# Kernel tuning notes

Measured on AMD Instinct MI355X. Metric: run time of the kernel, lower is better.

Reference implementation:

```python
import jax, jax.numpy as jnp
import numpy as np

B, S, D, H = 2, 2048, 1024, 16
DK = D // H


def setup_inputs() -> dict:
    key = jax.random.key(0)
    ks = jax.random.split(key, 12)
    scale = 1.0 / np.sqrt(D)
    inp = {
        "q": jax.random.normal(ks[0], (B, S, D), dtype=jnp.float32),
        "k": jax.random.normal(ks[1], (B, S, D), dtype=jnp.float32),
        "v": jax.random.normal(ks[2], (B, S, D), dtype=jnp.float32),
        "mask": jax.random.randint(ks[3], (B, 1, 1, S), 0, 2, dtype=jnp.int32),
        "Wq": jax.random.normal(ks[4], (D, D), dtype=jnp.float32) * scale,
        "bq": jnp.zeros((D,), dtype=jnp.float32),
        "Wk": jax.random.normal(ks[5], (D, D), dtype=jnp.float32) * scale,
        "bk": jnp.zeros((D,), dtype=jnp.float32),
        "Wv": jax.random.normal(ks[6], (D, D), dtype=jnp.float32) * scale,
        "bv": jnp.zeros((D,), dtype=jnp.float32),
        "Wo": jax.random.normal(ks[7], (D, D), dtype=jnp.float32) * scale,
        "bo": jnp.zeros((D,), dtype=jnp.float32),
    }
    return inp


def reference(q, k, v, mask, Wq, bq, Wk, bk, Wv, bv, Wo, bo):
    # Linear projections (torch nn.Linear: x @ W.T + b)
    query = q @ Wq.T + bq                      # [B,S,D]
    key = k @ Wk.T + bk
    value = v @ Wv.T + bv
    # split heads -> [B,H,S,DK]
    def split(x):
        return x.reshape(B, S, H, DK).transpose(0, 2, 1, 3)
    qh, kh, vh = split(query), split(key), split(value)
    # scaled dot-product attention with additive mask
    scores = jnp.einsum("bhqd,bhkd->bhqk", qh, kh) / jnp.sqrt(jnp.float32(DK))
    scores = jnp.where(mask == 0, jnp.float32(-1e9), scores)
    attn = jax.nn.softmax(scores, axis=-1)     # [B,H,S,S]
    out = jnp.einsum("bhqk,bhkd->bhqd", attn, vh)
    out = out.transpose(0, 2, 1, 3).reshape(B, S, D)
    return out @ Wo.T + bo
```

## Files before the change

kernel.cpp:

```cpp
#include <hip/hip_runtime.h>


constexpr int BB = 2;
constexpr int SS = 2048;
constexpr int DD = 1024;
constexpr int HH = 16;
constexpr int DKK = 64;

typedef float f32x4 __attribute__((ext_vector_type(4)));
typedef __bf16 bf16x8 __attribute__((ext_vector_type(8)));
typedef short s16x8 __attribute__((ext_vector_type(8)));
typedef short s16x4 __attribute__((ext_vector_type(4)));
typedef unsigned u32x2 __attribute__((ext_vector_type(2)));

#define DEV static __device__ __forceinline__

DEV f32x4 mfma16(s16x8 a, s16x8 b, f32x4 c) {
  return __builtin_amdgcn_mfma_f32_16x16x32_bf16(
      __builtin_bit_cast(bf16x8, a), __builtin_bit_cast(bf16x8, b), c, 0, 0, 0);
}

#if __has_builtin(__builtin_amdgcn_mfma_f32_16x16x16bf16_1k)
DEV f32x4 mfma16k(s16x4 a, s16x4 b, f32x4 c) {
  return __builtin_amdgcn_mfma_f32_16x16x16bf16_1k(a, b, c, 0, 0, 0);
}
#else
DEV f32x4 mfma16k(s16x4 a, s16x4 b, f32x4 c) {
  asm volatile(
      "s_nop 1\n\t"
      "v_mfma_f32_16x16x16_bf16 %0, %1, %2, %0\n\t"
      "s_nop 7\n\t"
      "s_nop 7"
      : "+v"(c)
      : "v"(a), "v"(b));
  return c;
}
#endif

DEV void split1(float x, short& h, short& l) {
  unsigned u = __float_as_uint(x);
  h = (short)(u >> 16);
  float hf = __uint_as_float(u & 0xffff0000u);
  l = (short)(__float_as_uint(x - hf) >> 16);
}
DEV short f2bf_rne(float x) {
  unsigned u = __float_as_uint(x);
  return (short)((u + 0x7fffu + ((u >> 16) & 1u)) >> 16);
}
DEV unsigned cvtpk(float lo, float hi) {
  unsigned r;
  asm("v_cvt_pk_bf16_f32 %0, %1, %2" : "=v"(r) : "v"(lo), "v"(hi));
  return r;
}
DEV s16x8 load8s(const short* p) { return *(const s16x8*)p; }

DEV void gld_lds16(const short* g, short* l) {
  __builtin_amdgcn_global_load_lds(
      (const __attribute__((address_space(1))) void*)g,
      (__attribute__((address_space(3))) void*)l, 16, 0, 0);
}

DEV void split4(const float* __restrict__ X, short* __restrict__ H,
                short* __restrict__ L, int i) {
  float4 x = *(const float4*)(X + i);
  float xs[4] = {x.x, x.y, x.z, x.w};
  s16x4 h4, l4;
#pragma unroll
  for (int e = 0; e < 4; ++e) {
    short h, l;
    split1(xs[e], h, l);
    h4[e] = h;
    l4[e] = l;
  }
  *(s16x4*)(H + i) = h4;
  *(s16x4*)(L + i) = l4;
}

DEV void cast4(const float* __restrict__ X, short* __restrict__ Y, int i) {
  float4 x = *(const float4*)(X + i);
  float xs[4] = {x.x, x.y, x.z, x.w};
  s16x4 y4;
#pragma unroll
  for (int e = 0; e < 4; ++e) y4[e] = f2bf_rne(xs[e]);
  *(s16x4*)(Y + i) = y4;
}

__global__ __launch_bounds__(256) void prep(
    const float* __restrict__ Wq, short* __restrict__ Wqh, short* __restrict__ Wql,
    const float* __restrict__ Wk, short* __restrict__ Wkh, short* __restrict__ Wkl,
    const float* __restrict__ Wo, short* __restrict__ Woh, short* __restrict__ Wol,
    const float* __restrict__ Wv, short* __restrict__ Wvh,
    const float* __restrict__ q, short* __restrict__ qH, short* __restrict__ qL,
    const float* __restrict__ k, short* __restrict__ kH, short* __restrict__ kL) {
  const int bid = blockIdx.x;
  const int t = threadIdx.x;
  if (bid < 4096) {
    const int w = bid >> 10;
    const int i = ((bid & 1023) * 256 + t) * 4;
    if (w == 0) split4(Wq, Wqh, Wql, i);
    else if (w == 1) split4(Wk, Wkh, Wkl, i);
    else if (w == 2) split4(Wo, Woh, Wol, i);
    else cast4(Wv, Wvh, i);
  } else {
    const int a = (bid - 4096) >> 12;
    const int i = (((bid - 4096) & 4095) * 256 + t) * 4;
    if (a == 0) split4(q, qH, qL, i);
    else split4(k, kH, kL, i);
  }
}

__global__ __launch_bounds__(256) void cast_rne(const float* __restrict__ X,
                                                short* __restrict__ Y) {
  int i = (blockIdx.x * 256 + threadIdx.x) * 4;
  cast4(X, Y, i);
}

__global__ __launch_bounds__(256) void gemm_qk(
    const short* __restrict__ qAh, const short* __restrict__ qAl,
    const short* __restrict__ Wqh, const short* __restrict__ Wql,
    const float* __restrict__ bq, short* __restrict__ Qo,
    const short* __restrict__ kAh, const short* __restrict__ kAl,
    const short* __restrict__ Wkh, const short* __restrict__ Wkl,
    const float* __restrict__ bk, short* __restrict__ Kho,
    short* __restrict__ Klo) {
  __shared__ short lds[2][12288];

  const int tid = threadIdx.x;
  const int lane = tid & 63, wv = tid >> 6;
  const int lo16 = lane & 15, quad = lane >> 4;
  const int sel = blockIdx.x >> 9;
  const int bid = blockIdx.x & 511;
  const int m0 = (bid & 31) * 128;
  const int n0 = (bid >> 5) * 64;

  const short* Agh = sel ? kAh : qAh;
  const short* Agl = sel ? kAl : qAl;
  const short* Wgh = sel ? Wkh : Wqh;
  const short* Wgl = sel ? Wkl : Wql;
  const float* bias = sel ? bk : bq;

  f32x4 acc[2][4];
#pragma unroll
  for (int mt = 0; mt < 2; ++mt)
#pragma unroll
    for (int nt = 0; nt < 4; ++nt) acc[mt][nt] = f32x4{0.f, 0.f, 0.f, 0.f};

  const int rw = tid >> 2, qw = tid & 3;
  const int ra0 = tid >> 2, ra1 = (tid + 256) >> 2;

  auto stage = [&](int k0, int buf) {
    short* sAh = lds[buf];
    short* sAl = lds[buf] + 4096;
    short* sWh = lds[buf] + 8192;
    short* sWl = lds[buf] + 10240;
    gld_lds16(Wgh + (size_t)(n0 + rw) * DD + k0 + qw * 8, sWh + tid * 8);
    gld_lds16(Wgl + (size_t)(n0 + rw) * DD + k0 + qw * 8, sWl + tid * 8);
    gld_lds16(Agh + (size_t)(m0 + ra0) * DD + k0 + qw * 8, sAh + tid * 8);
    gld_lds16(Agh + (size_t)(m0 + ra1) * DD + k0 + qw * 8, sAh + (tid + 256) * 8);
    gld_lds16(Agl + (size_t)(m0 + ra0) * DD + k0 + qw * 8, sAl + tid * 8);
    gld_lds16(Agl + (size_t)(m0 + ra1) * DD + k0 + qw * 8, sAl + (tid + 256) * 8);
  };

  stage(0, 0);

  for (int kk = 0; kk < DD / 32; ++kk) {
    __syncthreads();
    if (kk + 1 < DD / 32) stage((kk + 1) * 32, (kk + 1) & 1);

    const short* sAh = lds[kk & 1];
    const short* sAl = lds[kk & 1] + 4096;
    const short* sWh = lds[kk & 1] + 8192;
    const short* sWl = lds[kk & 1] + 10240;

    s16x8 ah[2], al[2], wh[4], wl[4];
#pragma unroll
    for (int mt = 0; mt < 2; ++mt) {
      const int r = wv * 32 + mt * 16 + lo16;
      ah[mt] = *(const s16x8*)&sAh[r * 32 + quad * 8];
      al[mt] = *(const s16x8*)&sAl[r * 32 + quad * 8];
    }
#pragma unroll
    for (int nt = 0; nt < 4; ++nt) {
      const int r = nt * 16 + lo16;
      wh[nt] = *(const s16x8*)&sWh[r * 32 + quad * 8];
      wl[nt] = *(const s16x8*)&sWl[r * 32 + quad * 8];
    }
#pragma unroll
    for (int mt = 0; mt < 2; ++mt)
#pragma unroll
      for (int nt = 0; nt < 4; ++nt) {
        acc[mt][nt] = mfma16(ah[mt], wh[nt], acc[mt][nt]);
        acc[mt][nt] = mfma16(ah[mt], wl[nt], acc[mt][nt]);
        acc[mt][nt] = mfma16(al[mt], wh[nt], acc[mt][nt]);
      }
  }

#pragma unroll
  for (int mt = 0; mt < 2; ++mt)
#pragma unroll
    for (int nt = 0; nt < 4; ++nt) {
      const int n = n0 + nt * 16 + lo16;
      const float bv = bias[n];
#pragma unroll
      for (int r = 0; r < 4; ++r) {
        const int m = m0 + wv * 32 + mt * 16 + quad * 4 + r;
        const float val = acc[mt][nt][r] + bv;
        const int b = m >> 11, s = m & 2047;
        const int h = n >> 6, dk = n & 63;
        if (sel == 0) {
          size_t idx = ((size_t)(b * HH + h) * SS + s) * DKK + dk;
          Qo[idx] = f2bf_rne(val);
        } else {
          const int dk_sw = dk ^ ((s & 7) << 3);
          size_t idx = ((size_t)(b * HH + h) * SS + s) * DKK + dk_sw;
          short hh, ll;
          split1(val, hh, ll);
          Kho[idx] = hh;
          Klo[idx] = ll;
        }
      }
    }
}

template <int SPLIT, int EPI>
__global__ __launch_bounds__(256) void gemm_tile(
    const short* __restrict__ Agh, const short* __restrict__ Agl,
    const short* __restrict__ Wgh, const short* __restrict__ Wgl,
    const float* __restrict__ bias, void* __restrict__ O1, void* __restrict__ O2) {
  __shared__ short lds[2][12288];

  const int tid = threadIdx.x;
  const int lane = tid & 63, wv = tid >> 6;
  const int lo16 = lane & 15, quad = lane >> 4;
  const int m0 = (blockIdx.x & 31) * 128;
  const int n0 = (blockIdx.x >> 5) * 64;

  f32x4 acc[2][4];
#pragma unroll
  for (int mt = 0; mt < 2; ++mt)
#pragma unroll
    for (int nt = 0; nt < 4; ++nt) acc[mt][nt] = f32x4{0.f, 0.f, 0.f, 0.f};

  const int rw = tid >> 2, qw = tid & 3;
  const int ra0 = tid >> 2, ra1 = (tid + 256) >> 2;

  auto stage = [&](int k0, int buf) {
    short* sAh = lds[buf];
    short* sAl = lds[buf] + 4096;
    short* sWh = lds[buf] + 8192;
    short* sWl = lds[buf] + 10240;
    gld_lds16(Wgh + (size_t)(n0 + rw) * DD + k0 + qw * 8, sWh + tid * 8);
    if constexpr (SPLIT)
      gld_lds16(Wgl + (size_t)(n0 + rw) * DD + k0 + qw * 8, sWl + tid * 8);
    gld_lds16(Agh + (size_t)(m0 + ra0) * DD + k0 + qw * 8, sAh + tid * 8);
    gld_lds16(Agh + (size_t)(m0 + ra1) * DD + k0 + qw * 8, sAh + (tid + 256) * 8);
    if constexpr (SPLIT) {
      gld_lds16(Agl + (size_t)(m0 + ra0) * DD + k0 + qw * 8, sAl + tid * 8);
      gld_lds16(Agl + (size_t)(m0 + ra1) * DD + k0 + qw * 8, sAl + (tid + 256) * 8);
    }
  };

  stage(0, 0);

  for (int kk = 0; kk < DD / 32; ++kk) {
    __syncthreads();
    if (kk + 1 < DD / 32) stage((kk + 1) * 32, (kk + 1) & 1);

    const short* sAh = lds[kk & 1];
    const short* sAl = lds[kk & 1] + 4096;
    const short* sWh = lds[kk & 1] + 8192;
    const short* sWl = lds[kk & 1] + 10240;

    s16x8 ah[2], al[2], wh[4], wl[4];
#pragma unroll
    for (int mt = 0; mt < 2; ++mt) {
      const int r = wv * 32 + mt * 16 + lo16;
      ah[mt] = *(const s16x8*)&sAh[r * 32 + quad * 8];
      if constexpr (SPLIT) al[mt] = *(const s16x8*)&sAl[r * 32 + quad * 8];
    }
#pragma unroll
    for (int nt = 0; nt < 4; ++nt) {
      const int r = nt * 16 + lo16;
      wh[nt] = *(const s16x8*)&sWh[r * 32 + quad * 8];
      if constexpr (SPLIT) wl[nt] = *(const s16x8*)&sWl[r * 32 + quad * 8];
    }
#pragma unroll
    for (int mt = 0; mt < 2; ++mt)
#pragma unroll
      for (int nt = 0; nt < 4; ++nt) {
        acc[mt][nt] = mfma16(ah[mt], wh[nt], acc[mt][nt]);
        if constexpr (SPLIT) {
          acc[mt][nt] = mfma16(ah[mt], wl[nt], acc[mt][nt]);
          acc[mt][nt] = mfma16(al[mt], wh[nt], acc[mt][nt]);
        }
      }
  }

#pragma unroll
  for (int mt = 0; mt < 2; ++mt)
#pragma unroll
    for (int nt = 0; nt < 4; ++nt) {
      const int n = n0 + nt * 16 + lo16;
      const float bv = bias[n];
#pragma unroll
      for (int r = 0; r < 4; ++r) {
        const int m = m0 + wv * 32 + mt * 16 + quad * 4 + r;
        const float val = acc[mt][nt][r] + bv;
        const int b = m >> 11, s = m & 2047;
        const int h = n >> 6, dk = n & 63;
        if constexpr (EPI == 1) {
          const int s_sw = s ^ ((dk & 3) << 4);
          size_t idx = ((size_t)(b * HH + h) * DKK + dk) * SS + s_sw;
          ((short*)O1)[idx] = f2bf_rne(val);
        } else {
          ((float*)O1)[(size_t)m * DD + n] = val;
        }
      }
    }
}

constexpr int NKB = SS / 64;
constexpr float EXPSC = 0.125f * 1.4426950408889634f;

__global__ __launch_bounds__(256, 2) void mha_attn(
    const short* __restrict__ Qh, const short* __restrict__ Kh,
    const short* __restrict__ Kl, const short* __restrict__ Vt,
    const int* __restrict__ mask, short* __restrict__ Ah,
    short* __restrict__ Al) {
  __shared__ __align__(16) short sKV[2][12288];

  const int tid = threadIdx.x;
  const int lane = tid & 63, wv = tid >> 6;
  const int lo16 = lane & 15, quad = lane >> 4;
  const int bid = blockIdx.x;
  const int head = (bid & 7) * 4 + ((bid >> 3) & 3);
  const int qblk = bid >> 5;
  const int q0 = qblk * 128 + wv * 32;
  const int b = head >> 4;

  const size_t hbase = (size_t)head * SS;
  const size_t vbase = (size_t)head * DKK;

  constexpr short ONE_BF = (short)0x3F80;
  const s16x4 ones4 = {ONE_BF, ONE_BF, ONE_BF, ONE_BF};

  s16x8 qh[2][2];
#pragma unroll
  for (int rt = 0; rt < 2; ++rt) {
    size_t qb = (hbase + q0 + rt * 16 + lo16) * DKK + quad * 8;
#pragma unroll
    for (int c = 0; c < 2; ++c) qh[rt][c] = load8s(Qh + qb + c * 32);
  }

  f32x4 Oacc[2][4];
#pragma unroll
  for (int rt = 0; rt < 2; ++rt)
#pragma unroll
    for (int t = 0; t < 4; ++t) Oacc[rt][t] = f32x4{0.f, 0.f, 0.f, 0.f};
  f32x4 sacc[2];
  sacc[0] = f32x4{0.f, 0.f, 0.f, 0.f};
  sacc[1] = f32x4{0.f, 0.f, 0.f, 0.f};

  auto STAGE = [&](int k0, int buf) {
    short* base = &sKV[buf][0];
#pragma unroll
    for (int i = 0; i < 2; ++i) {
      const int ch = tid + 256 * i;
      const int row = ch >> 3;
      const int inner = (ch & 7) * 8;
      gld_lds16(Kh + (hbase + k0 + row) * DKK + inner, base + ch * 8);
      gld_lds16(Kl + (hbase + k0 + row) * DKK + inner, base + 4096 + ch * 8);
      gld_lds16(Vt + (vbase + row) * SS + k0 + inner, base + 8192 + ch * 8);
    }
  };

  STAGE(0, 0);

  for (int kb = 0; kb < NKB; ++kb) {
    const int k0g = kb * 64;
    const int cur = kb & 1;
    __syncthreads();

    if (kb + 1 < NKB) STAGE(k0g + 64, cur ^ 1);

    const short* sKh = &sKV[cur][0];
    const short* sKl = &sKV[cur][4096];
    const short* sV = &sKV[cur][8192];

    float addf[4][4];
#pragma unroll
    for (int sub = 0; sub < 4; ++sub) {
      const int4 mq = *(const int4*)(mask + b * SS + k0g + sub * 16 + quad * 4);
      addf[sub][0] = mq.x ? 0.f : -32768.f;
      addf[sub][1] = mq.y ? 0.f : -32768.f;
      addf[sub][2] = mq.z ? 0.f : -32768.f;
      addf[sub][3] = mq.w ? 0.f : -32768.f;
    }

    f32x4 sc4[2][4];
    __builtin_amdgcn_s_setprio(1);
#pragma unroll
    for (int sub = 0; sub < 4; ++sub) {
      sc4[0][sub] = f32x4{0.f, 0.f, 0.f, 0.f};
      sc4[1][sub] = f32x4{0.f, 0.f, 0.f, 0.f};
      const int krow = sub * 16 + lo16;
      const int ksw = (krow & 7) << 3;
#pragma unroll
      for (int c = 0; c < 2; ++c) {
        const int koff = krow * 64 + ((c * 32 + quad * 8) ^ ksw);
        s16x8 kh = *(const s16x8*)&sKh[koff];
        s16x8 kl = *(const s16x8*)&sKl[koff];
#pragma unroll
        for (int rt = 0; rt < 2; ++rt) {
          sc4[rt][sub] = mfma16(kh, qh[rt][c], sc4[rt][sub]);
          sc4[rt][sub] = mfma16(kl, qh[rt][c], sc4[rt][sub]);
        }
      }
    }
    __builtin_amdgcn_s_setprio(0);

    s16x4 pb[2][4];
#pragma unroll
    for (int rt = 0; rt < 2; ++rt)
#pragma unroll
      for (int sub = 0; sub < 4; ++sub) {
        const float p0 = exp2f(fmaf(sc4[rt][sub][0], EXPSC, addf[sub][0]));
        const float p1 = exp2f(fmaf(sc4[rt][sub][1], EXPSC, addf[sub][1]));
        const float p2 = exp2f(fmaf(sc4[rt][sub][2], EXPSC, addf[sub][2]));
        const float p3 = exp2f(fmaf(sc4[rt][sub][3], EXPSC, addf[sub][3]));
        u32x2 w;
        w[0] = cvtpk(p0, p1);
        w[1] = cvtpk(p2, p3);
        pb[rt][sub] = __builtin_bit_cast(s16x4, w);
      }

    __builtin_amdgcn_s_setprio(1);
#pragma unroll
    for (int rt = 0; rt < 2; ++rt)
#pragma unroll
      for (int sub = 0; sub < 4; ++sub)
        sacc[rt] = mfma16k(ones4, pb[rt][sub], sacc[rt]);
#pragma unroll
    for (int t = 0; t < 4; ++t) {
      const int vrow = t * 16 + lo16;
      const int vsw = (lo16 & 3) << 4;
#pragma unroll
      for (int sub = 0; sub < 4; ++sub) {
        s16x4 va = *(const s16x4*)&sV[vrow * 64 + ((sub * 16 + quad * 4) ^ vsw)];
#pragma unroll
        for (int rt = 0; rt < 2; ++rt)
          Oacc[rt][t] = mfma16k(va, pb[rt][sub], Oacc[rt][t]);
      }
    }
    __builtin_amdgcn_s_setprio(0);
  }

  __syncthreads();
  float* sT = (float*)&sKV[0][0] + wv * (16 * 68);
  const int h = head & 15;
#pragma unroll
  for (int rt = 0; rt < 2; ++rt) {
    const float rinv = 1.0f / sacc[rt][0];
#pragma unroll
    for (int t = 0; t < 4; ++t) {
      f32x4 vv;
#pragma unroll
      for (int r = 0; r < 4; ++r) vv[r] = Oacc[rt][t][r] * rinv;
      *(f32x4*)&sT[lo16 * 68 + t * 16 + quad * 4] = vv;
    }
#pragma unroll
    for (int i = 0; i < 4; ++i) {
      const int qrow = quad + 4 * i;
      f32x4 vv = *(const f32x4*)&sT[qrow * 68 + lo16 * 4];
      const int row = q0 + rt * 16 + qrow;
      const size_t idx = ((size_t)b * SS + row) * DD + h * DKK + lo16 * 4;
      s16x4 hh, ll;
#pragma unroll
      for (int e = 0; e < 4; ++e) {
        short he, le;
        split1(vv[e], he, le);
        hh[e] = he;
        ll[e] = le;
      }
      *(s16x4*)&Ah[idx] = hh;
      *(s16x4*)&Al[idx] = ll;
    }
  }
}

extern "C" void kernel_launch(void* const* d_in, const int* in_sizes, int n_in,
                              void* d_out, int out_size, void* d_ws, size_t ws_size,
                              hipStream_t stream) {
  const float* q = (const float*)d_in[0];
  const float* k = (const float*)d_in[1];
  const float* v = (const float*)d_in[2];
  const int* mask = (const int*)d_in[3];
  const float* Wq = (const float*)d_in[4];
  const float* bq = (const float*)d_in[5];
  const float* Wk = (const float*)d_in[6];
  const float* bk = (const float*)d_in[7];
  const float* Wv = (const float*)d_in[8];
  const float* bv = (const float*)d_in[9];
  const float* Wo = (const float*)d_in[10];
  const float* bo = (const float*)d_in[11];

  char* ws = (char*)d_ws;
  size_t off = 0;
  auto take = [&](size_t bytes) {
    char* p = ws + off;
    off += (bytes + 255) & ~(size_t)255;
    return p;
  };
  const size_t WE = (size_t)DD * DD;
  const size_t TE = (size_t)BB * SS * DD;

  short* Wqh = (short*)take(WE * 2);
  short* Wql = (short*)take(WE * 2);
  short* Wkh = (short*)take(WE * 2);
  short* Wkl = (short*)take(WE * 2);
  short* Wvh = (short*)take(WE * 2);
  short* Woh = (short*)take(WE * 2);
  short* Wol = (short*)take(WE * 2);
  short* qH = (short*)take(TE * 2);
  short* qL = (short*)take(TE * 2);
  short* kH = (short*)take(TE * 2);
  short* kL = (short*)take(TE * 2);
  short* Qh = (short*)take(TE * 2);
  short* Kh = (short*)take(TE * 2);
  short* Kl = (short*)take(TE * 2);
  (void)ws_size;
  short* vH = qH;
  short* Vt = qL;
  short* aH = kH;
  short* aL = kL;

  prep<<<12288, 256, 0, stream>>>(Wq, Wqh, Wql, Wk, Wkh, Wkl, Wo, Woh, Wol,
                                  Wv, Wvh, q, qH, qL, k, kH, kL);

  gemm_qk<<<1024, 256, 0, stream>>>(qH, qL, Wqh, Wql, bq, Qh,
                                    kH, kL, Wkh, Wkl, bk, Kh, Kl);

  cast_rne<<<4096, 256, 0, stream>>>(v, vH);
  gemm_tile<0, 1><<<512, 256, 0, stream>>>(vH, nullptr, Wvh, nullptr, bv, Vt, nullptr);

  mha_attn<<<512, 256, 0, stream>>>(Qh, Kh, Kl, Vt, mask, aH, aL);

  gemm_tile<1, 2><<<512, 256, 0, stream>>>(aH, aL, Woh, Wol, bo, d_out, nullptr);
}
```

Before: 315.8 us.

## Store attention output as single bf16 and permute V layout for 128-bit LDS reads

The attention output is now written as one bf16 array instead of a hi/lo split pair. The output projection runs a new SPLIT=2 mode that keeps only the weight low part, which drops one of three MFMAs and one activation load stream. Separately, the V-transpose epilogue writes with a new permutation so the attention PV loop can do one 16-byte LDS read per two MFMAs instead of two 8-byte reads. The cost is lower precision on the attention output fed to the final GEMM.

```diff
diff --git a/kernel.cpp b/kernel.cpp
--- a/kernel.cpp
+++ b/kernel.cpp
@@ -58,6 +58,12 @@
   __builtin_amdgcn_global_load_lds(
       (const __attribute__((address_space(1))) void*)g,
       (__attribute__((address_space(3))) void*)l, 16, 0, 0);
+}
+
+DEV int vperm(int s_t, int d) {
+  const int sub = (s_t >> 4) & 3, qd = (s_t >> 2) & 3, j = s_t & 3;
+  const int slot = (((qd << 1) | (sub >> 1)) ^ (d & 7));
+  return (slot << 3) | ((sub & 1) << 2) | j;
 }
 
 DEV void split4(const float* __restrict__ X, short* __restrict__ H,
@@ -250,11 +256,11 @@
     short* sWh = lds[buf] + 8192;
     short* sWl = lds[buf] + 10240;
     gld_lds16(Wgh + (size_t)(n0 + rw) * DD + k0 + qw * 8, sWh + tid * 8);
-    if constexpr (SPLIT)
+    if constexpr (SPLIT >= 1)
       gld_lds16(Wgl + (size_t)(n0 + rw) * DD + k0 + qw * 8, sWl + tid * 8);
     gld_lds16(Agh + (size_t)(m0 + ra0) * DD + k0 + qw * 8, sAh + tid * 8);
     gld_lds16(Agh + (size_t)(m0 + ra1) * DD + k0 + qw * 8, sAh + (tid + 256) * 8);
-    if constexpr (SPLIT) {
+    if constexpr (SPLIT == 1) {
       gld_lds16(Agl + (size_t)(m0 + ra0) * DD + k0 + qw * 8, sAl + tid * 8);
       gld_lds16(Agl + (size_t)(m0 + ra1) * DD + k0 + qw * 8, sAl + (tid + 256) * 8);
     }
@@ -276,23 +282,23 @@
     for (int mt = 0; mt < 2; ++mt) {
       const int r = wv * 32 + mt * 16 + lo16;
       ah[mt] = *(const s16x8*)&sAh[r * 32 + quad * 8];
-      if constexpr (SPLIT) al[mt] = *(const s16x8*)&sAl[r * 32 + quad * 8];
+      if constexpr (SPLIT == 1) al[mt] = *(const s16x8*)&sAl[r * 32 + quad * 8];
     }
 #pragma unroll
     for (int nt = 0; nt < 4; ++nt) {
       const int r = nt * 16 + lo16;
       wh[nt] = *(const s16x8*)&sWh[r * 32 + quad * 8];
-      if constexpr (SPLIT) wl[nt] = *(const s16x8*)&sWl[r * 32 + quad * 8];
+      if constexpr (SPLIT >= 1) wl[nt] = *(const s16x8*)&sWl[r * 32 + quad * 8];
     }
 #pragma unroll
     for (int mt = 0; mt < 2; ++mt)
 #pragma unroll
       for (int nt = 0; nt < 4; ++nt) {
         acc[mt][nt] = mfma16(ah[mt], wh[nt], acc[mt][nt]);
-        if constexpr (SPLIT) {
+        if constexpr (SPLIT >= 1)
           acc[mt][nt] = mfma16(ah[mt], wl[nt], acc[mt][nt]);
+        if constexpr (SPLIT == 1)
           acc[mt][nt] = mfma16(al[mt], wh[nt], acc[mt][nt]);
-        }
       }
   }
 
@@ -309,8 +315,8 @@
         const int b = m >> 11, s = m & 2047;
         const int h = n >> 6, dk = n & 63;
         if constexpr (EPI == 1) {
-          const int s_sw = s ^ ((dk & 3) << 4);
-          size_t idx = ((size_t)(b * HH + h) * DKK + dk) * SS + s_sw;
+          const int col = (s & ~63) | vperm(s & 63, dk);
+          size_t idx = ((size_t)(b * HH + h) * DKK + dk) * SS + col;
           ((short*)O1)[idx] = f2bf_rne(val);
         } else {
           ((float*)O1)[(size_t)m * DD + n] = val;
@@ -325,8 +331,7 @@
 __global__ __launch_bounds__(256, 2) void mha_attn(
     const short* __restrict__ Qh, const short* __restrict__ Kh,
     const short* __restrict__ Kl, const short* __restrict__ Vt,
-    const int* __restrict__ mask, short* __restrict__ Ah,
-    short* __restrict__ Al) {
+    const int* __restrict__ mask, short* __restrict__ Ao) {
   __shared__ __align__(16) short sKV[2][12288];
 
   const int tid = threadIdx.x;
@@ -443,13 +448,17 @@
 #pragma unroll
     for (int t = 0; t < 4; ++t) {
       const int vrow = t * 16 + lo16;
-      const int vsw = (lo16 & 3) << 4;
-#pragma unroll
-      for (int sub = 0; sub < 4; ++sub) {
-        s16x4 va = *(const s16x4*)&sV[vrow * 64 + ((sub * 16 + quad * 4) ^ vsw)];
-#pragma unroll
-        for (int rt = 0; rt < 2; ++rt)
-          Oacc[rt][t] = mfma16k(va, pb[rt][sub], Oacc[rt][t]);
+#pragma unroll
+      for (int h2 = 0; h2 < 2; ++h2) {
+        const int slot = (((quad << 1) | h2) ^ (vrow & 7));
+        s16x8 va8 = *(const s16x8*)&sV[vrow * 64 + slot * 8];
+        s16x4 va0 = {va8[0], va8[1], va8[2], va8[3]};
+        s16x4 va1 = {va8[4], va8[5], va8[6], va8[7]};
+#pragma unroll
+        for (int rt = 0; rt < 2; ++rt) {
+          Oacc[rt][t] = mfma16k(va0, pb[rt][2 * h2], Oacc[rt][t]);
+          Oacc[rt][t] = mfma16k(va1, pb[rt][2 * h2 + 1], Oacc[rt][t]);
+        }
       }
     }
     __builtin_amdgcn_s_setprio(0);
@@ -474,16 +483,10 @@
       f32x4 vv = *(const f32x4*)&sT[qrow * 68 + lo16 * 4];
       const int row = q0 + rt * 16 + qrow;
       const size_t idx = ((size_t)b * SS + row) * DD + h * DKK + lo16 * 4;
-      s16x4 hh, ll;
-#pragma unroll
-      for (int e = 0; e < 4; ++e) {
-        short he, le;
-        split1(vv[e], he, le);
-        hh[e] = he;
-        ll[e] = le;
-      }
-      *(s16x4*)&Ah[idx] = hh;
-      *(s16x4*)&Al[idx] = ll;
+      u32x2 w;
+      w[0] = cvtpk(vv[0], vv[1]);
+      w[1] = cvtpk(vv[2], vv[3]);
+      *(s16x4*)&Ao[idx] = __builtin_bit_cast(s16x4, w);
     }
   }
 }
@@ -531,8 +534,7 @@
   (void)ws_size;
   short* vH = qH;
   short* Vt = qL;
-  short* aH = kH;
-  short* aL = kL;
+  short* Ao = kH;
 
   prep<<<12288, 256, 0, stream>>>(Wq, Wqh, Wql, Wk, Wkh, Wkl, Wo, Woh, Wol,
                                   Wv, Wvh, q, qH, qL, k, kH, kL);
@@ -543,7 +545,7 @@
   cast_rne<<<4096, 256, 0, stream>>>(v, vH);
   gemm_tile<0, 1><<<512, 256, 0, stream>>>(vH, nullptr, Wvh, nullptr, bv, Vt, nullptr);
 
-  mha_attn<<<512, 256, 0, stream>>>(Qh, Kh, Kl, Vt, mask, aH, aL);
-
-  gemm_tile<1, 2><<<512, 256, 0, stream>>>(aH, aL, Woh, Wol, bo, d_out, nullptr);
-}
+  mha_attn<<<512, 256, 0, stream>>>(Qh, Kh, Kl, Vt, mask, Ao);
+
+  gemm_tile<2, 2><<<512, 256, 0, stream>>>(Ao, nullptr, Woh, Wol, bo, d_out, nullptr);
+}
```

Result: faster. 291.8 us (-7.6%).
